# Kernel tuning notes

Hardware: AMD Instinct MI355X
Metric: run time of the kernel (lower is better)

Reference implementation:

```python
import jax, jax.numpy as jnp
import numpy as np

CHUNK = 256  # rows of the distance matrix materialized at a time


def _min_sq_dist(x, y):
    """For each point in x [N,3], squared distance to nearest point in y [M,3].
    Computed tile-by-tile via lax.scan so the full [N,M] matrix is never built.
    Matches pytorch3d knn_points(K=1).dists (squared Euclidean)."""
    n = x.shape[0]
    x2 = jnp.sum(x * x, axis=-1)            # [N]
    y2 = jnp.sum(y * y, axis=-1)            # [M]
    xs = x.reshape(n // CHUNK, CHUNK, 3)
    x2s = x2.reshape(n // CHUNK, CHUNK)

    def body(carry, inp):
        xc, x2c = inp                        # [C,3], [C]
        d = x2c[:, None] + y2[None, :] - 2.0 * (xc @ y.T)
        return carry, jnp.min(d, axis=1)     # [C]

    _, mins = jax.lax.scan(body, None, (xs, x2s))
    return mins.reshape(-1)                  # [N]


def setup_inputs() -> dict:
    key = jax.random.key(0)
    k1, k2 = jax.random.split(key)
    pred = jax.random.normal(k1, (131072, 4), dtype=jnp.float32)
    target = jax.random.normal(k2, (131072, 4), dtype=jnp.float32)
    return {"pred": pred, "target": target}


def reference(pred, target):
    loss_weight = 1.0
    p = pred[:, :3]
    t = target[:, :3]
    min_p2t = _min_sq_dist(p, t)   # adv_KNN: pred -> target
    min_t2p = _min_sq_dist(t, p)   # ori_KNN: target -> pred
    chamfer = jnp.mean(min_p2t) + jnp.mean(min_t2p)
    return chamfer * loss_weight
```

## Files before the change

kernel.cpp:

```cpp
#include <hip/hip_runtime.h>


#define G 128
#define GSH 7
#define CCELLS (G * G * G)
#define H 0.1f
#define INVH 10.0f
#define ORIG (-6.4f)
#define NCHUNK (CCELLS / 256)
#define SSTRIDE 2097168u

__device__ __forceinline__ int cellcoord(float x) {
    int c = (int)floorf((x - ORIG) * INVH);
    return min(max(c, 0), G - 1);
}
__device__ __forceinline__ int cellof(float x, float y, float z) {
    return (cellcoord(z) << (2 * GSH)) + (cellcoord(y) << GSH) + cellcoord(x);
}
__device__ __forceinline__ float axdist(int u, float qc) {
    float lo = ORIG + u * H;
    return fmaxf(0.0f, fmaxf(lo - qc, qc - (lo + H)));
}

__global__ __launch_bounds__(256) void hist2_kernel(
    const float4* __restrict__ A, const float4* __restrict__ B,
    unsigned int* __restrict__ counts, int n) {
    int i = blockIdx.x * 256 + threadIdx.x;
    const float4* in = blockIdx.y ? B : A;
    unsigned int* c = counts + blockIdx.y * CCELLS;
    if (i < n) {
        float4 a = in[i];
        atomicAdd(&c[cellof(a.x, a.y, a.z)], 1u);
    }
}

__global__ __launch_bounds__(256) void scan_chunk2_kernel(
    const unsigned int* __restrict__ counts, unsigned int* __restrict__ excl,
    unsigned int* __restrict__ blockSums) {
    __shared__ unsigned int lds[256];
    int cb = blockIdx.x & (NCHUNK - 1);
    int b = blockIdx.x >> 13;
    int g = cb * 256 + threadIdx.x;
    unsigned int v = counts[b * CCELLS + g];
    lds[threadIdx.x] = v;
    __syncthreads();
    for (int off = 1; off < 256; off <<= 1) {
        unsigned int t = (threadIdx.x >= off) ? lds[threadIdx.x - off] : 0u;
        __syncthreads();
        lds[threadIdx.x] += t;
        __syncthreads();
    }
    excl[b * SSTRIDE + g] = lds[threadIdx.x] - v;
    if (threadIdx.x == 255) blockSums[blockIdx.x] = lds[255];
}

__global__ __launch_bounds__(256) void scan_sums2_kernel(
    unsigned int* __restrict__ bs0) {
    unsigned int* bs = bs0 + blockIdx.x * NCHUNK;
    __shared__ unsigned int lds[256];
    int t = threadIdx.x;
    unsigned int s = 0;
    for (int k = 0; k < NCHUNK / 256; ++k) s += bs[t * (NCHUNK / 256) + k];
    lds[t] = s;
    __syncthreads();
    for (int off = 1; off < 256; off <<= 1) {
        unsigned int u = (t >= off) ? lds[t - off] : 0u;
        __syncthreads();
        lds[t] += u;
        __syncthreads();
    }
    unsigned int run = lds[t] - s;
    for (int k = 0; k < NCHUNK / 256; ++k) {
        unsigned int v = bs[t * (NCHUNK / 256) + k];
        bs[t * (NCHUNK / 256) + k] = run;
        run += v;
    }
}

__global__ __launch_bounds__(256) void add_offsets2_kernel(
    unsigned int* __restrict__ excl, const unsigned int* __restrict__ bs, int n) {
    int cb = blockIdx.x & (NCHUNK - 1);
    int b = blockIdx.x >> 13;
    int g = cb * 256 + threadIdx.x;
    excl[b * SSTRIDE + g] += bs[blockIdx.x];
    if (g == 0) excl[b * SSTRIDE + CCELLS] = (unsigned int)n;
}

__global__ __launch_bounds__(256) void copynext2_kernel(
    const unsigned int* __restrict__ excl, unsigned int* __restrict__ next) {
    int cb = blockIdx.x & (NCHUNK - 1);
    int b = blockIdx.x >> 13;
    int g = cb * 256 + threadIdx.x;
    next[b * CCELLS + g] = excl[b * SSTRIDE + g];
}

__global__ __launch_bounds__(256) void scatter2_kernel(
    const float4* __restrict__ A, const float4* __restrict__ B,
    unsigned int* __restrict__ next, float4* __restrict__ sorted, int n) {
    int i = blockIdx.x * 256 + threadIdx.x;
    const float4* in = blockIdx.y ? B : A;
    unsigned int* nx = next + blockIdx.y * CCELLS;
    float4* out = sorted + blockIdx.y * n;
    if (i < n) {
        float4 a = in[i];
        unsigned int slot = atomicAdd(&nx[cellof(a.x, a.y, a.z)], 1u);
        float s = fmaf(a.x, a.x, fmaf(a.y, a.y, a.z * a.z));
        out[slot] = make_float4(a.x, a.y, a.z, s);
    }
}

__global__ __launch_bounds__(256) void nn_pass1_kernel(
    const float4* __restrict__ Q, int nq,
    const unsigned int* __restrict__ start, const float4* __restrict__ pts,
    unsigned int* __restrict__ wl, unsigned int* __restrict__ cnt,
    double* __restrict__ acc) {
    int i = blockIdx.x * 256 + threadIdx.x;
    float v = 0.0f;
    if (i < nq) {
        float4 q = Q[i];
        float cx = -2.0f * q.x, cy = -2.0f * q.y, cz = -2.0f * q.z;
        float q2 = q.w;
        int qx = cellcoord(q.x), qy = cellcoord(q.y), qz = cellcoord(q.z);
        int x0 = max(qx - 1, 0), x1 = min(qx + 1, G - 1);
        unsigned int ss[9], ee[9];
        int idx = 0;
#pragma unroll
        for (int dz = -1; dz <= 1; ++dz) {
            int uz = min(max(qz + dz, 0), G - 1);
#pragma unroll
            for (int dy = -1; dy <= 1; ++dy) {
                int uy = min(max(qy + dy, 0), G - 1);
                unsigned int base = ((unsigned)uz << (2 * GSH)) + ((unsigned)uy << GSH);
                ss[idx] = start[base + x0];
                ee[idx] = start[base + x1 + 1];
                ++idx;
            }
        }
        float best = 3.4e38f;
#pragma unroll
        for (int r = 0; r < 9; ++r) {
            unsigned int k = ss[r], e = ee[r];
            for (; k + 2 <= e; k += 2) {
                float4 ya = pts[k];
                float4 yb = pts[k + 1];
                float ea = fmaf(cx, ya.x, fmaf(cy, ya.y, fmaf(cz, ya.z, ya.w)));
                float eb = fmaf(cx, yb.x, fmaf(cy, yb.y, fmaf(cz, yb.z, yb.w)));
                best = fminf(fminf(best, ea), eb);
            }
            if (k < e) {
                float4 ya = pts[k];
                best = fminf(best, fmaf(cx, ya.x, fmaf(cy, ya.y, fmaf(cz, ya.z, ya.w))));
            }
        }
        float ba = q2 + best;
        if (ba <= H * H) {
            v = ba;
        } else {
            unsigned int w = atomicAdd(cnt, 1u);
            wl[w] = (unsigned int)i;
        }
    }
    for (int off = 32; off > 0; off >>= 1) v += __shfl_down(v, off);
    __shared__ float partial[4];
    int lane = threadIdx.x & 63, wid = threadIdx.x >> 6;
    if (lane == 0) partial[wid] = v;
    __syncthreads();
    if (threadIdx.x == 0)
        atomicAdd(acc, (double)((partial[0] + partial[1]) + (partial[2] + partial[3])));
}

__global__ __launch_bounds__(256) void nn_pass2_kernel(
    const float4* __restrict__ Q,
    const unsigned int* __restrict__ start, const float4* __restrict__ pts,
    const unsigned int* __restrict__ wl, const unsigned int* __restrict__ cnt,
    double* __restrict__ acc) {
    int lane = threadIdx.x & 63;
    int gwave = (blockIdx.x * 256 + threadIdx.x) >> 6;
    int nwave = gridDim.x * 4;
    unsigned int m = *cnt;
    float wsum = 0.0f;
    for (unsigned int e = gwave; e < m; e += (unsigned int)nwave) {
        unsigned int qi = wl[e];
        float4 q = Q[qi];
        float cx = -2.0f * q.x, cy = -2.0f * q.y, cz = -2.0f * q.z;
        float q2 = q.w;
        int qx = cellcoord(q.x), qy = cellcoord(q.y), qz = cellcoord(q.z);
        float best = 3.4e38f;
        int Rb = 2;
        for (;;) {
            int z0 = max(qz - Rb, 0), z1 = min(qz + Rb, G - 1);
            int y0 = max(qy - Rb, 0), y1 = min(qy + Rb, G - 1);
            int x0 = max(qx - Rb, 0), x1 = min(qx + Rb, G - 1);
            int nyr = y1 - y0 + 1;
            int nrows = (z1 - z0 + 1) * nyr;
            float lbest = best;
            for (int r = lane; r < nrows; r += 64) {
                int uz = z0 + r / nyr;
                int uy = y0 + r % nyr;
                float dz = axdist(uz, q.z), dy = axdist(uy, q.y);
                float rowd2 = fmaf(dz, dz, dy * dy);
                if (rowd2 >= q2 + lbest) continue;
                unsigned int base = ((unsigned)uz << (2 * GSH)) + ((unsigned)uy << GSH);
                unsigned int k = start[base + x0], ke = start[base + x1 + 1];
                for (; k < ke; ++k) {
                    float4 ya = pts[k];
                    lbest = fminf(lbest,
                        fmaf(cx, ya.x, fmaf(cy, ya.y, fmaf(cz, ya.z, ya.w))));
                }
            }
            for (int off = 32; off > 0; off >>= 1)
                lbest = fminf(lbest, __shfl_xor(lbest, off));
            best = lbest;
            float bnd = (float)Rb * H;
            if (bnd * bnd >= q2 + best || Rb >= G) break;
            Rb = min(Rb * 2, G);
        }
        wsum += q2 + best;
    }
    if (lane == 0) atomicAdd(acc, (double)wsum);
}

__global__ void finalize_kernel(const double* __restrict__ acc,
                                float* __restrict__ out, int n) {
    out[0] = (float)(acc[0] / (double)n);
}

#define SPLIT 16
#define PTS 4
__global__ __launch_bounds__(256) void pack_kernel(
    const float4* __restrict__ in, float4* __restrict__ out, int n) {
    int i = blockIdx.x * 256 + threadIdx.x;
    if (i < n) {
        float4 a = in[i];
        float s = fmaf(a.x, a.x, fmaf(a.y, a.y, a.z * a.z));
        out[i] = make_float4(a.x, a.y, a.z, s);
    }
}
__device__ __forceinline__ unsigned int enc_f32(float f) {
    unsigned int u = __float_as_uint(f);
    return (u & 0x80000000u) ? ~u : (u | 0x80000000u);
}
__device__ __forceinline__ float dec_f32(unsigned int u) {
    u = (u & 0x80000000u) ? (u ^ 0x80000000u) : ~u;
    return __uint_as_float(u);
}
__global__ __launch_bounds__(256) void chamfer_dir_kernel(
    const float4* __restrict__ X, const float4* __restrict__ Y,
    int m, unsigned int* __restrict__ mins) {
    int base = blockIdx.x * (256 * PTS) + threadIdx.x;
    float x2x[PTS], x2y[PTS], x2z[PTS], xw[PTS], mn[PTS];
#pragma unroll
    for (int p = 0; p < PTS; ++p) {
        float4 x = X[base + p * 256];
        x2x[p] = -2.0f * x.x; x2y[p] = -2.0f * x.y; x2z[p] = -2.0f * x.z;
        xw[p] = x.w; mn[p] = 3.4e38f;
    }
    int seglen = m / SPLIT, j0 = blockIdx.y * seglen, j1 = j0 + seglen;
    for (int j = j0; j < j1; j += 8) {
#pragma unroll
        for (int u = 0; u < 8; u += 2) {
            float4 ya = Y[j + u];
            float4 yb = Y[j + u + 1];
#pragma unroll
            for (int p = 0; p < PTS; ++p) {
                float ea = fmaf(x2x[p], ya.x, fmaf(x2y[p], ya.y, fmaf(x2z[p], ya.z, ya.w)));
                float eb = fmaf(x2x[p], yb.x, fmaf(x2y[p], yb.y, fmaf(x2z[p], yb.z, yb.w)));
                mn[p] = fminf(fminf(mn[p], ea), eb);
            }
        }
    }
#pragma unroll
    for (int p = 0; p < PTS; ++p)
        atomicMin(&mins[base + p * 256], enc_f32(xw[p] + mn[p]));
}
__global__ __launch_bounds__(256) void reduce_kernel(
    const unsigned int* __restrict__ mins, int total, double* __restrict__ acc) {
    float s = 0.0f;
    for (int i = blockIdx.x * 256 + threadIdx.x; i < total; i += gridDim.x * 256)
        s += dec_f32(mins[i]);
    for (int off = 32; off > 0; off >>= 1) s += __shfl_down(s, off);
    __shared__ float partial[4];
    int lane = threadIdx.x & 63, wid = threadIdx.x >> 6;
    if (lane == 0) partial[wid] = s;
    __syncthreads();
    if (threadIdx.x == 0)
        atomicAdd(acc, (double)((partial[0] + partial[1]) + (partial[2] + partial[3])));
}

extern "C" void kernel_launch(void* const* d_in, const int* in_sizes, int n_in,
                              void* d_out, int out_size, void* d_ws, size_t ws_size,
                              hipStream_t stream) {
    const float4* pred = (const float4*)d_in[0];
    const float4* targ = (const float4*)d_in[1];
    float* out = (float*)d_out;
    int n = in_sizes[0] / 4;
    int nblk = (n + 255) / 256;

    char* ws = (char*)d_ws;
    double* acc = (double*)ws;
    unsigned int* cntP = (unsigned int*)(ws + 8);
    unsigned int* cntT = (unsigned int*)(ws + 12);

    size_t startB = (size_t)SSTRIDE * 4;
    size_t needGrid = 64 + 2 * startB + 2ull * CCELLS * 4 + 2ull * n * 16
                    + 2ull * NCHUNK * 4;

    if (ws_size >= needGrid && n == 131072) {
        char* p = ws + 64;
        unsigned int* startPT = (unsigned int*)p;  p += 2 * startB;
        unsigned int* nextPT = (unsigned int*)p;   p += 2ull * CCELLS * 4;
        float4* sortedPT = (float4*)p;             p += 2ull * n * 16;
        unsigned int* blockSums = (unsigned int*)p;
        unsigned int* startP = startPT;
        unsigned int* startT = startPT + SSTRIDE;
        float4* sortedP = sortedPT;
        float4* sortedT = sortedPT + n;
        unsigned int* wlP = nextPT;
        unsigned int* wlT = nextPT + CCELLS;

        hipMemsetAsync(ws, 0, 16, stream);
        hipMemsetAsync(nextPT, 0, 2ull * CCELLS * 4, stream);
        hist2_kernel<<<dim3(nblk, 2), 256, 0, stream>>>(pred, targ, nextPT, n);
        scan_chunk2_kernel<<<2 * NCHUNK, 256, 0, stream>>>(nextPT, startPT, blockSums);
        scan_sums2_kernel<<<2, 256, 0, stream>>>(blockSums);
        add_offsets2_kernel<<<2 * NCHUNK, 256, 0, stream>>>(startPT, blockSums, n);
        copynext2_kernel<<<2 * NCHUNK, 256, 0, stream>>>(startPT, nextPT);
        scatter2_kernel<<<dim3(nblk, 2), 256, 0, stream>>>(pred, targ, nextPT, sortedPT, n);

        nn_pass1_kernel<<<nblk, 256, 0, stream>>>(sortedP, n, startT, sortedT, wlP, cntP, acc);
        nn_pass1_kernel<<<nblk, 256, 0, stream>>>(sortedT, n, startP, sortedP, wlT, cntT, acc);
        nn_pass2_kernel<<<256, 256, 0, stream>>>(sortedP, startT, sortedT, wlP, cntP, acc);
        nn_pass2_kernel<<<256, 256, 0, stream>>>(sortedT, startP, sortedP, wlT, cntT, acc);
    } else {
        hipMemsetAsync(acc, 0, sizeof(double), stream);
        size_t needBF = 64 + 2ull * n * sizeof(float4) + 2ull * n * sizeof(unsigned int);
        if (ws_size >= needBF && (n % (256 * PTS)) == 0 && (n % SPLIT) == 0) {
            float4* P = (float4*)(ws + 64);
            float4* T = P + n;
            unsigned int* minPT = (unsigned int*)(T + n);
            pack_kernel<<<nblk, 256, 0, stream>>>(pred, P, n);
            pack_kernel<<<nblk, 256, 0, stream>>>(targ, T, n);
            hipMemsetAsync(minPT, 0xFF, 2ull * n * sizeof(unsigned int), stream);
            dim3 grid(n / (256 * PTS), SPLIT);
            chamfer_dir_kernel<<<grid, 256, 0, stream>>>(P, T, n, minPT);
            chamfer_dir_kernel<<<grid, 256, 0, stream>>>(T, P, n, minPT + n);
            reduce_kernel<<<256, 256, 0, stream>>>(minPT, 2 * n, acc);
        }
    }
    finalize_kernel<<<1, 1, 0, stream>>>(acc, out, n);
}
```

Baseline: 256.9 us.

## Shrink grid to 64^3, fuse scan copy, merge direction launches, seed pass2

Shrinks the uniform grid from 128^3 to 64^3 cells over a smaller extent, and makes boundary cells unbounded in the axis lower-bound distance so points outside the extent stay correct. This cuts the cost of the histogram, scan and offset passes, which scale with the cell count. The copy-to-next kernel is folded into add_offsets, and both search directions run in single 2-D launches for pass1 and pass2. Pass1 now stores its partial best for points it defers, and pass2 starts from that value, with a larger pass2 grid. The risks are more outliers clamped into boundary cells and longer fallback searches for them.

```diff
diff --git a/kernel.cpp b/kernel.cpp
--- a/kernel.cpp
+++ b/kernel.cpp
@@ -1,14 +1,14 @@
 #include <hip/hip_runtime.h>
 
 
-#define G 128
-#define GSH 7
+#define G 64
+#define GSH 6
 #define CCELLS (G * G * G)
 #define H 0.1f
 #define INVH 10.0f
-#define ORIG (-6.4f)
+#define ORIG (-3.2f)
 #define NCHUNK (CCELLS / 256)
-#define SSTRIDE 2097168u
+#define SSTRIDE 262160u
 
 __device__ __forceinline__ int cellcoord(float x) {
     int c = (int)floorf((x - ORIG) * INVH);
@@ -19,7 +19,9 @@
 }
 __device__ __forceinline__ float axdist(int u, float qc) {
     float lo = ORIG + u * H;
-    return fmaxf(0.0f, fmaxf(lo - qc, qc - (lo + H)));
+    float dlo = (u == 0) ? 0.0f : lo - qc;
+    float dhi = (u == G - 1) ? 0.0f : qc - (lo + H);
+    return fmaxf(0.0f, fmaxf(dlo, dhi));
 }
 
 __global__ __launch_bounds__(256) void hist2_kernel(
@@ -39,7 +41,7 @@
     unsigned int* __restrict__ blockSums) {
     __shared__ unsigned int lds[256];
     int cb = blockIdx.x & (NCHUNK - 1);
-    int b = blockIdx.x >> 13;
+    int b = blockIdx.x >> 10;
     int g = cb * 256 + threadIdx.x;
     unsigned int v = counts[b * CCELLS + g];
     lds[threadIdx.x] = v;
@@ -60,6 +62,7 @@
     __shared__ unsigned int lds[256];
     int t = threadIdx.x;
     unsigned int s = 0;
+#pragma unroll
     for (int k = 0; k < NCHUNK / 256; ++k) s += bs[t * (NCHUNK / 256) + k];
     lds[t] = s;
     __syncthreads();
@@ -78,20 +81,15 @@
 }
 
 __global__ __launch_bounds__(256) void add_offsets2_kernel(
-    unsigned int* __restrict__ excl, const unsigned int* __restrict__ bs, int n) {
+    unsigned int* __restrict__ excl, unsigned int* __restrict__ next,
+    const unsigned int* __restrict__ bs, int n) {
     int cb = blockIdx.x & (NCHUNK - 1);
-    int b = blockIdx.x >> 13;
+    int b = blockIdx.x >> 10;
     int g = cb * 256 + threadIdx.x;
-    excl[b * SSTRIDE + g] += bs[blockIdx.x];
+    unsigned int v = excl[b * SSTRIDE + g] + bs[blockIdx.x];
+    excl[b * SSTRIDE + g] = v;
+    next[b * CCELLS + g] = v;
     if (g == 0) excl[b * SSTRIDE + CCELLS] = (unsigned int)n;
-}
-
-__global__ __launch_bounds__(256) void copynext2_kernel(
-    const unsigned int* __restrict__ excl, unsigned int* __restrict__ next) {
-    int cb = blockIdx.x & (NCHUNK - 1);
-    int b = blockIdx.x >> 13;
-    int g = cb * 256 + threadIdx.x;
-    next[b * CCELLS + g] = excl[b * SSTRIDE + g];
 }
 
 __global__ __launch_bounds__(256) void scatter2_kernel(
@@ -110,13 +108,20 @@
 }
 
 __global__ __launch_bounds__(256) void nn_pass1_kernel(
-    const float4* __restrict__ Q, int nq,
-    const unsigned int* __restrict__ start, const float4* __restrict__ pts,
-    unsigned int* __restrict__ wl, unsigned int* __restrict__ cnt,
-    double* __restrict__ acc) {
+    const float4* __restrict__ sortedPT, const unsigned int* __restrict__ startPT,
+    int n, unsigned int* __restrict__ wlPT, unsigned int* __restrict__ wbPT,
+    unsigned int* __restrict__ cnts, double* __restrict__ acc) {
+    int dir = blockIdx.y;
+    const float4* Q = sortedPT + (size_t)dir * n;
+    const float4* pts = sortedPT + (size_t)(1 - dir) * n;
+    const unsigned int* start = startPT + (size_t)(1 - dir) * SSTRIDE;
+    unsigned int* wl = wlPT + (size_t)dir * n;
+    unsigned int* wb = wbPT + (size_t)dir * n;
+    unsigned int* cnt = cnts + dir;
+
     int i = blockIdx.x * 256 + threadIdx.x;
     float v = 0.0f;
-    if (i < nq) {
+    if (i < n) {
         float4 q = Q[i];
         float cx = -2.0f * q.x, cy = -2.0f * q.y, cz = -2.0f * q.z;
         float q2 = q.w;
@@ -158,6 +163,7 @@
         } else {
             unsigned int w = atomicAdd(cnt, 1u);
             wl[w] = (unsigned int)i;
+            wb[w] = __float_as_uint(best);
         }
     }
     for (int off = 32; off > 0; off >>= 1) v += __shfl_down(v, off);
@@ -170,14 +176,20 @@
 }
 
 __global__ __launch_bounds__(256) void nn_pass2_kernel(
-    const float4* __restrict__ Q,
-    const unsigned int* __restrict__ start, const float4* __restrict__ pts,
-    const unsigned int* __restrict__ wl, const unsigned int* __restrict__ cnt,
-    double* __restrict__ acc) {
+    const float4* __restrict__ sortedPT, const unsigned int* __restrict__ startPT,
+    int n, const unsigned int* __restrict__ wlPT, const unsigned int* __restrict__ wbPT,
+    const unsigned int* __restrict__ cnts, double* __restrict__ acc) {
+    int dir = blockIdx.y;
+    const float4* Q = sortedPT + (size_t)dir * n;
+    const float4* pts = sortedPT + (size_t)(1 - dir) * n;
+    const unsigned int* start = startPT + (size_t)(1 - dir) * SSTRIDE;
+    const unsigned int* wl = wlPT + (size_t)dir * n;
+    const unsigned int* wb = wbPT + (size_t)dir * n;
+    unsigned int m = cnts[dir];
+
     int lane = threadIdx.x & 63;
     int gwave = (blockIdx.x * 256 + threadIdx.x) >> 6;
     int nwave = gridDim.x * 4;
-    unsigned int m = *cnt;
     float wsum = 0.0f;
     for (unsigned int e = gwave; e < m; e += (unsigned int)nwave) {
         unsigned int qi = wl[e];
@@ -185,7 +197,7 @@
         float cx = -2.0f * q.x, cy = -2.0f * q.y, cz = -2.0f * q.z;
         float q2 = q.w;
         int qx = cellcoord(q.x), qy = cellcoord(q.y), qz = cellcoord(q.z);
-        float best = 3.4e38f;
+        float best = __uint_as_float(wb[e]);
         int Rb = 2;
         for (;;) {
             int z0 = max(qz - Rb, 0), z1 = min(qz + Rb, G - 1);
@@ -217,7 +229,7 @@
         }
         wsum += q2 + best;
     }
-    if (lane == 0) atomicAdd(acc, (double)wsum);
+    if (lane == 0 && wsum != 0.0f) atomicAdd(acc, (double)wsum);
 }
 
 __global__ void finalize_kernel(const double* __restrict__ acc,
@@ -298,39 +310,33 @@
 
     char* ws = (char*)d_ws;
     double* acc = (double*)ws;
-    unsigned int* cntP = (unsigned int*)(ws + 8);
-    unsigned int* cntT = (unsigned int*)(ws + 12);
+    unsigned int* cnts = (unsigned int*)(ws + 8);
 
     size_t startB = (size_t)SSTRIDE * 4;
     size_t needGrid = 64 + 2 * startB + 2ull * CCELLS * 4 + 2ull * n * 16
-                    + 2ull * NCHUNK * 4;
+                    + 4ull * n * 4 + 2ull * NCHUNK * 4;
 
     if (ws_size >= needGrid && n == 131072) {
         char* p = ws + 64;
         unsigned int* startPT = (unsigned int*)p;  p += 2 * startB;
         unsigned int* nextPT = (unsigned int*)p;   p += 2ull * CCELLS * 4;
         float4* sortedPT = (float4*)p;             p += 2ull * n * 16;
+        unsigned int* wlPT = (unsigned int*)p;     p += 2ull * n * 4;
+        unsigned int* wbPT = (unsigned int*)p;     p += 2ull * n * 4;
         unsigned int* blockSums = (unsigned int*)p;
-        unsigned int* startP = startPT;
-        unsigned int* startT = startPT + SSTRIDE;
-        float4* sortedP = sortedPT;
-        float4* sortedT = sortedPT + n;
-        unsigned int* wlP = nextPT;
-        unsigned int* wlT = nextPT + CCELLS;
 
         hipMemsetAsync(ws, 0, 16, stream);
         hipMemsetAsync(nextPT, 0, 2ull * CCELLS * 4, stream);
         hist2_kernel<<<dim3(nblk, 2), 256, 0, stream>>>(pred, targ, nextPT, n);
         scan_chunk2_kernel<<<2 * NCHUNK, 256, 0, stream>>>(nextPT, startPT, blockSums);
         scan_sums2_kernel<<<2, 256, 0, stream>>>(blockSums);
-        add_offsets2_kernel<<<2 * NCHUNK, 256, 0, stream>>>(startPT, blockSums, n);
-        copynext2_kernel<<<2 * NCHUNK, 256, 0, stream>>>(startPT, nextPT);
+        add_offsets2_kernel<<<2 * NCHUNK, 256, 0, stream>>>(startPT, nextPT, blockSums, n);
         scatter2_kernel<<<dim3(nblk, 2), 256, 0, stream>>>(pred, targ, nextPT, sortedPT, n);
 
-        nn_pass1_kernel<<<nblk, 256, 0, stream>>>(sortedP, n, startT, sortedT, wlP, cntP, acc);
-        nn_pass1_kernel<<<nblk, 256, 0, stream>>>(sortedT, n, startP, sortedP, wlT, cntT, acc);
-        nn_pass2_kernel<<<256, 256, 0, stream>>>(sortedP, startT, sortedT, wlP, cntP, acc);
-        nn_pass2_kernel<<<256, 256, 0, stream>>>(sortedT, startP, sortedP, wlT, cntT, acc);
+        nn_pass1_kernel<<<dim3(nblk, 2), 256, 0, stream>>>(
+            sortedPT, startPT, n, wlPT, wbPT, cnts, acc);
+        nn_pass2_kernel<<<dim3(2048, 2), 256, 0, stream>>>(
+            sortedPT, startPT, n, wlPT, wbPT, cnts, acc);
     } else {
         hipMemsetAsync(acc, 0, sizeof(double), stream);
         size_t needBF = 64 + 2ull * n * sizeof(float4) + 2ull * n * sizeof(unsigned int);
```

Result: slower. 333.2 us (+29.7%).
